# Optimization experiments

Measured on AMD Instinct MI355X. Metric: run time of the kernel, lower is better.

The kernel has to match this reference:

```python
import jax, jax.numpy as jnp
import numpy as np

MIN_VALUE = 0.01

def setup_inputs() -> dict:
    key = jax.random.key(0)
    kx, kw, kb = jax.random.split(key, 3)
    n_samples, n_channels, n_assets = 4096, 32, 500
    x = jax.random.normal(kx, (n_samples, n_channels, n_assets), dtype=jnp.float32)
    # nn.Linear(n_channels, 1): weight (1, n_channels), bias (1,)
    bound = 1.0 / np.sqrt(n_channels)
    W = jax.random.uniform(kw, (1, n_channels), dtype=jnp.float32, minval=-bound, maxval=bound)
    b = jax.random.uniform(kb, (1,), dtype=jnp.float32, minval=-bound, maxval=bound)
    return {"x": x, "W": W, "b": b}

def reference(x, W, b):
    # Fused equivalent of the per-(sample, asset) nn.Linear loop:
    # y[s, a] = sum_c W[0, c] * x[s, c, a] + b[0]
    y = jnp.einsum('sca,c->sa', x, W[0]) + b[0]          # (n_samples, n_assets)
    return jnp.mean(jnp.abs(y), axis=-1) + MIN_VALUE      # (n_samples,)
```

## Files before the change

kernel.cpp:

```cpp
#include <hip/hip_runtime.h>

#define NS 4096
#define NC 32
#define NA 500
#define NV 125
#define MIN_VALUE 0.01f

__global__ __launch_bounds__(128) void gamma_obo_kernel(
    const float* __restrict__ x,
    const float* __restrict__ W,
    const float* __restrict__ b,
    float* __restrict__ out)
{
    const int s = blockIdx.x;
    const int t = threadIdx.x;

    float w[NC];
#pragma unroll
    for (int c = 0; c < NC; ++c) w[c] = W[c];
    const float bias = b[0];

    float partial = 0.0f;
    if (t < NV) {
        const float4* __restrict__ xrow =
            (const float4*)(x + (size_t)s * (NC * NA));
        float4 acc = make_float4(bias, bias, bias, bias);
#pragma unroll
        for (int c = 0; c < NC; ++c) {
            float4 v = xrow[c * NV + t];
            acc.x = fmaf(w[c], v.x, acc.x);
            acc.y = fmaf(w[c], v.y, acc.y);
            acc.z = fmaf(w[c], v.z, acc.z);
            acc.w = fmaf(w[c], v.w, acc.w);
        }
        partial = fabsf(acc.x) + fabsf(acc.y) + fabsf(acc.z) + fabsf(acc.w);
    }

#pragma unroll
    for (int off = 32; off > 0; off >>= 1)
        partial += __shfl_down(partial, off, 64);

    __shared__ float smem[2];
    if ((t & 63) == 0) smem[t >> 6] = partial;
    __syncthreads();

    if (t == 0) {
        float total = smem[0] + smem[1];
        out[s] = total / (float)NA + MIN_VALUE;
    }
}

extern "C" void kernel_launch(void* const* d_in, const int* in_sizes, int n_in,
                              void* d_out, int out_size, void* d_ws, size_t ws_size,
                              hipStream_t stream) {
    const float* x = (const float*)d_in[0];
    const float* W = (const float*)d_in[1];
    const float* b = (const float*)d_in[2];
    float* out = (float*)d_out;
    gamma_obo_kernel<<<NS, 128, 0, stream>>>(x, W, b, out);
}
```

Before: 352.3 us.

## Use one wavefront per sample and drop shared-memory reduction

Each sample's row is now handled by a single 64-thread wavefront, with each lane processing up to two float4 columns. The cross-wave shared-memory reduction and __syncthreads are removed, leaving a pure xor-shuffle reduction. This cuts sync overhead and idle lanes, and gives more independent loads per thread. The trade-off is fewer resident threads per block, so load-level parallelism per sample relies on the unrolled loops. The kernel is memory bound, about 262 MB read.

```diff
diff --git a/kernel.cpp b/kernel.cpp
--- a/kernel.cpp
+++ b/kernel.cpp
@@ -6,7 +6,7 @@
 #define NV 125
 #define MIN_VALUE 0.01f
 
-__global__ __launch_bounds__(128) void gamma_obo_kernel(
+__global__ __launch_bounds__(64) void gamma_obo_kernel(
     const float* __restrict__ x,
     const float* __restrict__ W,
     const float* __restrict__ b,
@@ -20,34 +20,39 @@
     for (int c = 0; c < NC; ++c) w[c] = W[c];
     const float bias = b[0];
 
-    float partial = 0.0f;
-    if (t < NV) {
-        const float4* __restrict__ xrow =
-            (const float4*)(x + (size_t)s * (NC * NA));
-        float4 acc = make_float4(bias, bias, bias, bias);
+    const float4* __restrict__ xrow =
+        (const float4*)(x + (size_t)s * (NC * NA));
+
+    float4 acc0 = make_float4(bias, bias, bias, bias);
+#pragma unroll
+    for (int c = 0; c < NC; ++c) {
+        float4 v = xrow[c * NV + t];
+        acc0.x = fmaf(w[c], v.x, acc0.x);
+        acc0.y = fmaf(w[c], v.y, acc0.y);
+        acc0.z = fmaf(w[c], v.z, acc0.z);
+        acc0.w = fmaf(w[c], v.w, acc0.w);
+    }
+    float partial = fabsf(acc0.x) + fabsf(acc0.y) + fabsf(acc0.z) + fabsf(acc0.w);
+
+    if (t < NV - 64) {
+        float4 acc1 = make_float4(bias, bias, bias, bias);
 #pragma unroll
         for (int c = 0; c < NC; ++c) {
-            float4 v = xrow[c * NV + t];
-            acc.x = fmaf(w[c], v.x, acc.x);
-            acc.y = fmaf(w[c], v.y, acc.y);
-            acc.z = fmaf(w[c], v.z, acc.z);
-            acc.w = fmaf(w[c], v.w, acc.w);
+            float4 v = xrow[c * NV + 64 + t];
+            acc1.x = fmaf(w[c], v.x, acc1.x);
+            acc1.y = fmaf(w[c], v.y, acc1.y);
+            acc1.z = fmaf(w[c], v.z, acc1.z);
+            acc1.w = fmaf(w[c], v.w, acc1.w);
         }
-        partial = fabsf(acc.x) + fabsf(acc.y) + fabsf(acc.z) + fabsf(acc.w);
+        partial += fabsf(acc1.x) + fabsf(acc1.y) + fabsf(acc1.z) + fabsf(acc1.w);
     }
 
 #pragma unroll
-    for (int off = 32; off > 0; off >>= 1)
-        partial += __shfl_down(partial, off, 64);
+    for (int mask = 32; mask > 0; mask >>= 1)
+        partial += __shfl_xor(partial, mask, 64);
 
-    __shared__ float smem[2];
-    if ((t & 63) == 0) smem[t >> 6] = partial;
-    __syncthreads();
-
-    if (t == 0) {
-        float total = smem[0] + smem[1];
-        out[s] = total / (float)NA + MIN_VALUE;
-    }
+    if (t == 0)
+        out[s] = partial * (1.0f / (float)NA) + MIN_VALUE;
 }
 
 extern "C" void kernel_launch(void* const* d_in, const int* in_sizes, int n_in,
@@ -57,5 +62,5 @@
     const float* W = (const float*)d_in[1];
     const float* b = (const float*)d_in[2];
     float* out = (float*)d_out;
-    gamma_obo_kernel<<<NS, 128, 0, stream>>>(x, W, b, out);
+    gamma_obo_kernel<<<NS, 64, 0, stream>>>(x, W, b, out);
 }
```

Result: no change. 355.5 us (+0.9%).
